# Kernel tuning notes

Hardware: AMD Instinct MI355X
Metric: run time of the kernel (lower is better)

Reference implementation:

```python
import jax, jax.numpy as jnp
from jax import lax
import numpy as np

B, C, H, W = 16, 32, 256, 256
K = 3  # kernel size, padding=1 -> SAME


def setup_inputs() -> dict:
    key = jax.random.key(0)
    k1, k2, k3, k4, k5, k6 = jax.random.split(key, 6)
    x = jax.random.normal(k1, (B, C, H, W), dtype=jnp.float32)
    gate_values = jax.random.uniform(k2, (B, C), dtype=jnp.float32)
    # Stacked per-output-channel Conv2d experts == one [C, C, K, K] conv (OIHW)
    fan_in = C * K * K
    bound = 1.0 / np.sqrt(fan_in)
    w1 = jax.random.uniform(k3, (C, C, K, K), minval=-bound, maxval=bound, dtype=jnp.float32)
    b1 = jax.random.uniform(k4, (C,), minval=-bound, maxval=bound, dtype=jnp.float32)
    w2 = jax.random.uniform(k5, (C, C, K, K), minval=-bound, maxval=bound, dtype=jnp.float32)
    b2 = jax.random.uniform(k6, (C,), minval=-bound, maxval=bound, dtype=jnp.float32)
    return {"x": x, "gate_values": gate_values, "w1": w1, "b1": b1, "w2": w2, "b2": b2}


def _moe_conv(x, w, b, g):
    # x: [B,C,H,W], w: [C,C,K,K] (OIHW), b: [C], g: [B,C] effective gate
    y = lax.conv_general_dilated(
        x, w, window_strides=(1, 1), padding='SAME',
        dimension_numbers=('NCHW', 'OIHW', 'NCHW'))
    y = y + b[None, :, None, None]
    return y * g[:, :, None, None]


def reference(x, gate_values, w1, b1, w2, b2):
    # gate rows with value <= 0 are never written -> output stays zero;
    # selected rows are multiplied by the gate value (bias included).
    g = gate_values * (gate_values > 0).astype(gate_values.dtype)
    h = jax.nn.relu(_moe_conv(x, w1, b1, g))
    h = jax.nn.relu(_moe_conv(h, w2, b2, g))
    return h + x
```

## Files before the change

### kernel.cpp

```cpp
#include <hip/hip_runtime.h>

#define BB 16
#define CC 32
#define HH 256
#define WW 256

#define TW 32
#define TH 8
#define CIP 36

typedef short bf16x8 __attribute__((ext_vector_type(8)));
typedef float f32x16 __attribute__((ext_vector_type(16)));

struct alignas(8)  U2 { unsigned x, y; };
struct alignas(16) U4 { U2 lo, hi; };

__device__ __forceinline__ unsigned short f2bf(float f) {
    unsigned u = __float_as_uint(f);
    u += 0x7fffu + ((u >> 16) & 1u);
    return (unsigned short)(u >> 16);
}

__global__ void wprep(const float* __restrict__ w1, const float* __restrict__ w2,
                      unsigned short* __restrict__ wq) {
    int idx = blockIdx.x * 256 + threadIdx.x;
    if (idx >= 18 * 2 * 32 * 8) return;
    int j    = idx & 7;
    int n    = (idx >> 3) & 31;
    int half = (idx >> 8) & 1;
    int st   = idx >> 9;
    int s = st & 1, pos = st >> 1;
    int ci = s * 16 + half * 8 + j;
    int src = (n * CC + ci) * 9 + pos;
    wq[idx]        = f2bf(w1[src]);
    wq[9216 + idx] = f2bf(w2[src]);
}

template<bool FIRST>
__global__ __launch_bounds__(256)
void conv_mfma(const void* __restrict__ in,
               const unsigned short* __restrict__ wq,
               const float* __restrict__ bias,
               const float* __restrict__ gate,
               const float* __restrict__ resid,
               void* __restrict__ out)
{
    __shared__ unsigned short xs[TH + 2][TW + 2][CIP];
    __shared__ float gs[CC], bs[CC];

    const int t  = threadIdx.x;
    const int b  = blockIdx.z;
    const int y0 = blockIdx.y * TH;
    const int x0 = blockIdx.x * TW;

    if (t < CC) {
        float gv = gate[b * CC + t];
        gs[t] = gv > 0.f ? gv : 0.f;
        bs[t] = bias[t];
    }

    const int lane = t & 63;
    const int wv   = t >> 6;
    const int col  = lane & 31;
    const int half = lane >> 5;

    bf16x8 wf[18];
    #pragma unroll
    for (int st = 0; st < 18; ++st) {
        U4 w = ((const U4*)wq)[(st * 2 + half) * 32 + col];
        wf[st] = __builtin_bit_cast(bf16x8, w);
    }

    if (FIRST) {
        const float* x = (const float*)in;
        for (int idx = t; idx < CC * (TH + 2) * (TW + 2); idx += 256) {
            int ci  = idx / ((TH + 2) * (TW + 2));
            int rem = idx - ci * ((TH + 2) * (TW + 2));
            int y   = rem / (TW + 2);
            int xx  = rem - y * (TW + 2);
            int gy = y0 + y - 1, gx = x0 + xx - 1;
            float v = 0.f;
            if (gy >= 0 && gy < HH && gx >= 0 && gx < WW)
                v = x[(((size_t)b * CC + ci) * HH + gy) * WW + gx];
            xs[y][xx][ci] = f2bf(v);
        }
    } else {
        const unsigned short* h = (const unsigned short*)in;
        for (int idx = t; idx < (TH + 2) * (TW + 2) * 4; idx += 256) {
            int q = idx & 3;
            int p = idx >> 2;
            int y  = p / (TW + 2);
            int xx = p - y * (TW + 2);
            int gy = y0 + y - 1, gx = x0 + xx - 1;
            U4 v; v.lo = {0u, 0u}; v.hi = {0u, 0u};
            if (gy >= 0 && gy < HH && gx >= 0 && gx < WW)
                v = *(const U4*)(h + (((size_t)b * HH + gy) * WW + gx) * CC + q * 8);
            *(U2*)&xs[y][xx][q * 8]     = v.lo;
            *(U2*)&xs[y][xx][q * 8 + 4] = v.hi;
        }
    }
    __syncthreads();

    f32x16 acc0 = {0,0,0,0,0,0,0,0,0,0,0,0,0,0,0,0};
    f32x16 acc1 = {0,0,0,0,0,0,0,0,0,0,0,0,0,0,0,0};
    const int r0 = wv * 2, r1 = wv * 2 + 1;

    #pragma unroll
    for (int st = 0; st < 18; ++st) {
        const int pos = st >> 1, s = st & 1;
        const int kh = pos / 3, kw = pos - kh * 3;
        const int ci0 = s * 16 + half * 8;
        U4 xa, xb;
        xa.lo = *(const U2*)&xs[r0 + kh][col + kw][ci0];
        xa.hi = *(const U2*)&xs[r0 + kh][col + kw][ci0 + 4];
        xb.lo = *(const U2*)&xs[r1 + kh][col + kw][ci0];
        xb.hi = *(const U2*)&xs[r1 + kh][col + kw][ci0 + 4];
        acc0 = __builtin_amdgcn_mfma_f32_32x32x16_bf16(wf[st], __builtin_bit_cast(bf16x8, xa), acc0, 0, 0, 0);
        acc1 = __builtin_amdgcn_mfma_f32_32x32x16_bf16(wf[st], __builtin_bit_cast(bf16x8, xb), acc1, 0, 0, 0);
    }

    if (FIRST) {
        unsigned short* o = (unsigned short*)out;
        size_t p0 = (((size_t)b * HH + y0 + r0) * WW + x0 + col) * CC;
        size_t p1 = (((size_t)b * HH + y0 + r1) * WW + x0 + col) * CC;
        #pragma unroll
        for (int reg = 0; reg < 16; ++reg) {
            int co = (reg & 3) + 8 * (reg >> 2) + 4 * half;
            float v0 = (acc0[reg] + bs[co]) * gs[co]; v0 = v0 > 0.f ? v0 : 0.f;
            float v1 = (acc1[reg] + bs[co]) * gs[co]; v1 = v1 > 0.f ? v1 : 0.f;
            o[p0 + co] = f2bf(v0);
            o[p1 + co] = f2bf(v1);
        }
    } else {
        float* o = (float*)out;
        #pragma unroll
        for (int reg = 0; reg < 16; ++reg) {
            int co = (reg & 3) + 8 * (reg >> 2) + 4 * half;
            size_t i0 = (((size_t)b * CC + co) * HH + y0 + r0) * WW + x0 + col;
            size_t i1 = (((size_t)b * CC + co) * HH + y0 + r1) * WW + x0 + col;
            float v0 = (acc0[reg] + bs[co]) * gs[co];
            float v1 = (acc1[reg] + bs[co]) * gs[co];
            o[i0] = fmaxf(v0, 0.f) + resid[i0];
            o[i1] = fmaxf(v1, 0.f) + resid[i1];
        }
    }
}

extern "C" void kernel_launch(void* const* d_in, const int* in_sizes, int n_in,
                              void* d_out, int out_size, void* d_ws, size_t ws_size,
                              hipStream_t stream) {
    const float* x  = (const float*)d_in[0];
    const float* gv = (const float*)d_in[1];
    const float* w1 = (const float*)d_in[2];
    const float* b1 = (const float*)d_in[3];
    const float* w2 = (const float*)d_in[4];
    const float* b2 = (const float*)d_in[5];
    float* out = (float*)d_out;

    unsigned short* h1 = (unsigned short*)d_ws;
    unsigned short* wq = h1 + (size_t)BB * HH * WW * CC;

    wprep<<<36, 256, 0, stream>>>(w1, w2, wq);

    dim3 grid(WW / TW, HH / TH, BB);
    conv_mfma<true ><<<grid, 256, 0, stream>>>(x,  wq,        b1, gv, nullptr, h1);
    conv_mfma<false><<<grid, 256, 0, stream>>>(h1, wq + 9216, b2, gv, x,       out);
}
```

Before: 378.8 us.

## Loop each block over four row tiles and rework staging and bf16 packing

Each block now processes NT=4 consecutive row tiles, so the weight fragments are loaded once per four tiles. The next tile's staging is issued before the current tile's epilogue stores, overlapping global loads with output writes. The first-conv staging now loads 16 channels per pixel per thread and packs bf16 pairs with v_cvt_pk_bf16_f32. The first-conv epilogue also writes vectorised 8-byte stores instead of scalar shorts. The grid shrinks fourfold, which lowers parallelism and occupancy-driven latency hiding, and halo rows are still reloaded for every tile.

```diff
diff --git a/kernel.cpp b/kernel.cpp
--- a/kernel.cpp
+++ b/kernel.cpp
@@ -7,6 +7,7 @@
 
 #define TW 32
 #define TH 8
+#define NT 4
 #define CIP 36
 
 typedef short bf16x8 __attribute__((ext_vector_type(8)));
@@ -19,6 +20,12 @@
     unsigned u = __float_as_uint(f);
     u += 0x7fffu + ((u >> 16) & 1u);
     return (unsigned short)(u >> 16);
+}
+
+__device__ __forceinline__ unsigned cvtpk(float lo, float hi) {
+    unsigned r;
+    asm("v_cvt_pk_bf16_f32 %0, %1, %2" : "=v"(r) : "v"(lo), "v"(hi));
+    return r;
 }
 
 __global__ void wprep(const float* __restrict__ w1, const float* __restrict__ w2,
@@ -37,6 +44,62 @@
 }
 
 template<bool FIRST>
+__device__ __forceinline__ void stage_tile(const void* __restrict__ in, int b, int y0, int x0, int t,
+                                           unsigned short (&xs)[TH + 2][TW + 2][CIP])
+{
+    if (FIRST) {
+        const float* xb = (const float*)in + (size_t)b * CC * HH * WW;
+        #pragma unroll
+        for (int rep = 0; rep < 2; ++rep) {
+            int p = rep * 256 + t;
+            if (p < (TH + 2) * (TW + 2)) {
+                int y  = p / (TW + 2);
+                int xx = p - y * (TW + 2);
+                int gy = y0 + y - 1, gx = x0 + xx - 1;
+                bool inb = (gy >= 0 && gy < HH && gx >= 0 && gx < WW);
+                int off = gy * WW + gx;
+                #pragma unroll
+                for (int c16 = 0; c16 < 2; ++c16) {
+                    float v[16];
+                    #pragma unroll
+                    for (int j = 0; j < 16; ++j) v[j] = 0.f;
+                    if (inb) {
+                        #pragma unroll
+                        for (int j = 0; j < 16; ++j)
+                            v[j] = xb[(c16 * 16 + j) * (HH * WW) + off];
+                    }
+                    #pragma unroll
+                    for (int k = 0; k < 4; ++k) {
+                        U2 w;
+                        w.x = cvtpk(v[4 * k + 0], v[4 * k + 1]);
+                        w.y = cvtpk(v[4 * k + 2], v[4 * k + 3]);
+                        *(U2*)&xs[y][xx][c16 * 16 + k * 4] = w;
+                    }
+                }
+            }
+        }
+    } else {
+        const unsigned short* hb = (const unsigned short*)in + (size_t)b * HH * WW * CC;
+        #pragma unroll
+        for (int rep = 0; rep < 6; ++rep) {
+            int idx = rep * 256 + t;
+            if (idx < (TH + 2) * (TW + 2) * 4) {
+                int q = idx & 3;
+                int p = idx >> 2;
+                int y  = p / (TW + 2);
+                int xx = p - y * (TW + 2);
+                int gy = y0 + y - 1, gx = x0 + xx - 1;
+                U4 v; v.lo = {0u, 0u}; v.hi = {0u, 0u};
+                if (gy >= 0 && gy < HH && gx >= 0 && gx < WW)
+                    v = *(const U4*)(hb + ((gy * WW + gx) * CC + q * 8));
+                *(U2*)&xs[y][xx][q * 8]     = v.lo;
+                *(U2*)&xs[y][xx][q * 8 + 4] = v.hi;
+            }
+        }
+    }
+}
+
+template<bool FIRST>
 __global__ __launch_bounds__(256)
 void conv_mfma(const void* __restrict__ in,
                const unsigned short* __restrict__ wq,
@@ -48,10 +111,10 @@
     __shared__ unsigned short xs[TH + 2][TW + 2][CIP];
     __shared__ float gs[CC], bs[CC];
 
-    const int t  = threadIdx.x;
-    const int b  = blockIdx.z;
-    const int y0 = blockIdx.y * TH;
-    const int x0 = blockIdx.x * TW;
+    const int t     = threadIdx.x;
+    const int b     = blockIdx.z;
+    const int x0    = blockIdx.x * TW;
+    const int ybase = blockIdx.y * (TH * NT);
 
     if (t < CC) {
         float gv = gate[b * CC + t];
@@ -63,6 +126,7 @@
     const int wv   = t >> 6;
     const int col  = lane & 31;
     const int half = lane >> 5;
+    const int r0 = wv * 2, r1 = wv * 2 + 1;
 
     bf16x8 wf[18];
     #pragma unroll
@@ -71,77 +135,66 @@
         wf[st] = __builtin_bit_cast(bf16x8, w);
     }
 
-    if (FIRST) {
-        const float* x = (const float*)in;
-        for (int idx = t; idx < CC * (TH + 2) * (TW + 2); idx += 256) {
-            int ci  = idx / ((TH + 2) * (TW + 2));
-            int rem = idx - ci * ((TH + 2) * (TW + 2));
-            int y   = rem / (TW + 2);
-            int xx  = rem - y * (TW + 2);
-            int gy = y0 + y - 1, gx = x0 + xx - 1;
-            float v = 0.f;
-            if (gy >= 0 && gy < HH && gx >= 0 && gx < WW)
-                v = x[(((size_t)b * CC + ci) * HH + gy) * WW + gx];
-            xs[y][xx][ci] = f2bf(v);
-        }
-    } else {
-        const unsigned short* h = (const unsigned short*)in;
-        for (int idx = t; idx < (TH + 2) * (TW + 2) * 4; idx += 256) {
-            int q = idx & 3;
-            int p = idx >> 2;
-            int y  = p / (TW + 2);
-            int xx = p - y * (TW + 2);
-            int gy = y0 + y - 1, gx = x0 + xx - 1;
-            U4 v; v.lo = {0u, 0u}; v.hi = {0u, 0u};
-            if (gy >= 0 && gy < HH && gx >= 0 && gx < WW)
-                v = *(const U4*)(h + (((size_t)b * HH + gy) * WW + gx) * CC + q * 8);
-            *(U2*)&xs[y][xx][q * 8]     = v.lo;
-            *(U2*)&xs[y][xx][q * 8 + 4] = v.hi;
-        }
-    }
-    __syncthreads();
-
-    f32x16 acc0 = {0,0,0,0,0,0,0,0,0,0,0,0,0,0,0,0};
-    f32x16 acc1 = {0,0,0,0,0,0,0,0,0,0,0,0,0,0,0,0};
-    const int r0 = wv * 2, r1 = wv * 2 + 1;
-
-    #pragma unroll
-    for (int st = 0; st < 18; ++st) {
-        const int pos = st >> 1, s = st & 1;
-        const int kh = pos / 3, kw = pos - kh * 3;
-        const int ci0 = s * 16 + half * 8;
-        U4 xa, xb;
-        xa.lo = *(const U2*)&xs[r0 + kh][col + kw][ci0];
-        xa.hi = *(const U2*)&xs[r0 + kh][col + kw][ci0 + 4];
-        xb.lo = *(const U2*)&xs[r1 + kh][col + kw][ci0];
-        xb.hi = *(const U2*)&xs[r1 + kh][col + kw][ci0 + 4];
-        acc0 = __builtin_amdgcn_mfma_f32_32x32x16_bf16(wf[st], __builtin_bit_cast(bf16x8, xa), acc0, 0, 0, 0);
-        acc1 = __builtin_amdgcn_mfma_f32_32x32x16_bf16(wf[st], __builtin_bit_cast(bf16x8, xb), acc1, 0, 0, 0);
-    }
-
-    if (FIRST) {
-        unsigned short* o = (unsigned short*)out;
-        size_t p0 = (((size_t)b * HH + y0 + r0) * WW + x0 + col) * CC;
-        size_t p1 = (((size_t)b * HH + y0 + r1) * WW + x0 + col) * CC;
+    stage_tile<FIRST>(in, b, ybase, x0, t, xs);
+
+    #pragma unroll 1
+    for (int s = 0; s < NT; ++s) {
+        const int y0 = ybase + s * TH;
+        __syncthreads();
+
+        f32x16 acc0 = {0,0,0,0,0,0,0,0,0,0,0,0,0,0,0,0};
+        f32x16 acc1 = {0,0,0,0,0,0,0,0,0,0,0,0,0,0,0,0};
         #pragma unroll
-        for (int reg = 0; reg < 16; ++reg) {
-            int co = (reg & 3) + 8 * (reg >> 2) + 4 * half;
-            float v0 = (acc0[reg] + bs[co]) * gs[co]; v0 = v0 > 0.f ? v0 : 0.f;
-            float v1 = (acc1[reg] + bs[co]) * gs[co]; v1 = v1 > 0.f ? v1 : 0.f;
-            o[p0 + co] = f2bf(v0);
-            o[p1 + co] = f2bf(v1);
-        }
-    } else {
-        float* o = (float*)out;
-        #pragma unroll
-        for (int reg = 0; reg < 16; ++reg) {
-            int co = (reg & 3) + 8 * (reg >> 2) + 4 * half;
-            size_t i0 = (((size_t)b * CC + co) * HH + y0 + r0) * WW + x0 + col;
-            size_t i1 = (((size_t)b * CC + co) * HH + y0 + r1) * WW + x0 + col;
-            float v0 = (acc0[reg] + bs[co]) * gs[co];
-            float v1 = (acc1[reg] + bs[co]) * gs[co];
-            o[i0] = fmaxf(v0, 0.f) + resid[i0];
-            o[i1] = fmaxf(v1, 0.f) + resid[i1];
+        for (int st = 0; st < 18; ++st) {
+            const int pos = st >> 1, sb = st & 1;
+            const int kh = pos / 3, kw = pos - kh * 3;
+            const int ci0 = sb * 16 + half * 8;
+            U4 xa, xb;
+            xa.lo = *(const U2*)&xs[r0 + kh][col + kw][ci0];
+            xa.hi = *(const U2*)&xs[r0 + kh][col + kw][ci0 + 4];
+            xb.lo = *(const U2*)&xs[r1 + kh][col + kw][ci0];
+            xb.hi = *(const U2*)&xs[r1 + kh][col + kw][ci0 + 4];
+            acc0 = __builtin_amdgcn_mfma_f32_32x32x16_bf16(wf[st], __builtin_bit_cast(bf16x8, xa), acc0, 0, 0, 0);
+            acc1 = __builtin_amdgcn_mfma_f32_32x32x16_bf16(wf[st], __builtin_bit_cast(bf16x8, xb), acc1, 0, 0, 0);
+        }
+
+        __syncthreads();
+
+        if (s + 1 < NT) stage_tile<FIRST>(in, b, y0 + TH, x0, t, xs);
+
+        if (FIRST) {
+            unsigned short* ob = (unsigned short*)out + (size_t)b * HH * WW * CC;
+            int p0 = ((y0 + r0) * WW + x0 + col) * CC;
+            int p1 = ((y0 + r1) * WW + x0 + col) * CC;
+            #pragma unroll
+            for (int g = 0; g < 4; ++g) {
+                int c0 = 8 * g + 4 * half;
+                float a0 = fmaxf((acc0[4 * g + 0] + bs[c0 + 0]) * gs[c0 + 0], 0.f);
+                float a1 = fmaxf((acc0[4 * g + 1] + bs[c0 + 1]) * gs[c0 + 1], 0.f);
+                float a2 = fmaxf((acc0[4 * g + 2] + bs[c0 + 2]) * gs[c0 + 2], 0.f);
+                float a3 = fmaxf((acc0[4 * g + 3] + bs[c0 + 3]) * gs[c0 + 3], 0.f);
+                U2 w0; w0.x = cvtpk(a0, a1); w0.y = cvtpk(a2, a3);
+                *(U2*)(ob + p0 + c0) = w0;
+                float c0v = fmaxf((acc1[4 * g + 0] + bs[c0 + 0]) * gs[c0 + 0], 0.f);
+                float c1v = fmaxf((acc1[4 * g + 1] + bs[c0 + 1]) * gs[c0 + 1], 0.f);
+                float c2v = fmaxf((acc1[4 * g + 2] + bs[c0 + 2]) * gs[c0 + 2], 0.f);
+                float c3v = fmaxf((acc1[4 * g + 3] + bs[c0 + 3]) * gs[c0 + 3], 0.f);
+                U2 w1; w1.x = cvtpk(c0v, c1v); w1.y = cvtpk(c2v, c3v);
+                *(U2*)(ob + p1 + c0) = w1;
+            }
+        } else {
+            float* ob = (float*)out + (size_t)b * CC * HH * WW;
+            const float* rb = resid + (size_t)b * CC * HH * WW;
+            #pragma unroll
+            for (int reg = 0; reg < 16; ++reg) {
+                int co = (reg & 3) + 8 * (reg >> 2) + 4 * half;
+                int i0 = (co * HH + y0 + r0) * WW + x0 + col;
+                int i1 = (co * HH + y0 + r1) * WW + x0 + col;
+                float v0 = (acc0[reg] + bs[co]) * gs[co];
+                float v1 = (acc1[reg] + bs[co]) * gs[co];
+                ob[i0] = fmaxf(v0, 0.f) + rb[i0];
+                ob[i1] = fmaxf(v1, 0.f) + rb[i1];
+            }
         }
     }
 }
@@ -162,7 +215,7 @@
 
     wprep<<<36, 256, 0, stream>>>(w1, w2, wq);
 
-    dim3 grid(WW / TW, HH / TH, BB);
+    dim3 grid(WW / TW, HH / (TH * NT), BB);
     conv_mfma<true ><<<grid, 256, 0, stream>>>(x,  wq,        b1, gv, nullptr, h1);
     conv_mfma<false><<<grid, 256, 0, stream>>>(h1, wq + 9216, b2, gv, x,       out);
 }
```

New measurement: 336.5 us. 1.13x faster.
